# Kernel tuning notes

Hardware: AMD Instinct MI355X
Metric: run time of the kernel (lower is better)

Reference implementation:

```python
import jax, jax.numpy as jnp
import numpy as np

B, I, H = 131072, 128, 128


def _xavier(key, shape):
    fan_in, fan_out = shape
    limit = float(np.sqrt(6.0 / (fan_in + fan_out)))
    return jax.random.uniform(key, shape, jnp.float32, -limit, limit)


def setup_inputs() -> dict:
    key = jax.random.key(0)
    ks = jax.random.split(key, 12)
    inp = {
        "x_t": jax.random.normal(ks[0], (B, I), jnp.float32),
        "h_prev": jax.random.normal(ks[1], (B, H), jnp.float32),
        "c_prev": jax.random.normal(ks[2], (B, H), jnp.float32),
        "w_ii": _xavier(ks[3], (I, H)),
        "w_if": _xavier(ks[4], (I, H)),
        "w_ig": _xavier(ks[5], (I, H)),
        "w_io": _xavier(ks[6], (I, H)),
        "w_hi": _xavier(ks[7], (H, H)),
        "w_hf": _xavier(ks[8], (H, H)),
        "w_hg": _xavier(ks[9], (H, H)),
        "w_ho": _xavier(ks[10], (H, H)),
        "b_i": jnp.zeros((H,), jnp.float32),
        "b_f": jnp.zeros((H,), jnp.float32),
        "b_g": jnp.zeros((H,), jnp.float32),
        "b_o": jnp.zeros((H,), jnp.float32),
    }
    return inp


def reference(x_t, h_prev, c_prev, w_ii, w_if, w_ig, w_io,
              w_hi, w_hf, w_hg, w_ho, b_i, b_f, b_g, b_o):
    # Fused gate pre-activations: stack the 4 input and 4 hidden weight mats
    # so the 8 small GEMMs become 2 GEMMs of width 4H (same math as kernel).
    Wx = jnp.concatenate([w_ii, w_if, w_ig, w_io], axis=1)  # (I, 4H)
    Wh = jnp.concatenate([w_hi, w_hf, w_hg, w_ho], axis=1)  # (H, 4H)
    b = jnp.concatenate([b_i, b_f, b_g, b_o], axis=0)       # (4H,)
    acc = x_t @ Wx + h_prev @ Wh + b                         # (B, 4H)
    a_i, a_f, a_g, a_o = jnp.split(acc, 4, axis=1)
    i_gate = jax.nn.sigmoid(a_i)
    f_gate = jax.nn.sigmoid(a_f)
    o_gate = jax.nn.sigmoid(a_o)
    g_gate = jnp.tanh(a_g)
    c_t = f_gate * c_prev + i_gate * g_gate
    h_t = o_gate * jnp.tanh(c_t)
    return h_t, c_t
```

## Files before the change

### kernel.cpp

```cpp
#include <hip/hip_runtime.h>
#include <hip/hip_bf16.h>

#define BROWS 131072
#define HD 128

typedef __attribute__((ext_vector_type(8))) short bf16x8;
typedef __attribute__((ext_vector_type(4))) float f32x4;

static __device__ __forceinline__ unsigned short f2bf(float f) {
    union { float f; unsigned int i; } v;
    v.f = f;
    unsigned int u = v.i;
    u += 0x7FFFu + ((u >> 16) & 1u);
    return (unsigned short)(u >> 16);
}
static __device__ __forceinline__ float fast_sigmoid(float x) {
    float e = __builtin_amdgcn_exp2f(-1.442695040888963f * x);
    return __builtin_amdgcn_rcpf(1.0f + e);
}
static __device__ __forceinline__ float fast_tanh(float x) {
    float e = __builtin_amdgcn_exp2f(2.885390081777927f * x);
    return 1.0f - 2.0f * __builtin_amdgcn_rcpf(1.0f + e);
}

static __device__ __forceinline__ bf16x8 cvt8(const float* p) {
    f32x4 a = ((const f32x4*)p)[0];
    f32x4 b = ((const f32x4*)p)[1];
    __hip_bfloat162 r0 = __float22bfloat162_rn(float2{a[0], a[1]});
    __hip_bfloat162 r1 = __float22bfloat162_rn(float2{a[2], a[3]});
    __hip_bfloat162 r2 = __float22bfloat162_rn(float2{b[0], b[1]});
    __hip_bfloat162 r3 = __float22bfloat162_rn(float2{b[2], b[3]});
    union { __hip_bfloat162 h2; unsigned int u; } u0, u1, u2, u3;
    u0.h2 = r0; u1.h2 = r1; u2.h2 = r2; u3.h2 = r3;
    union { unsigned int u[4]; bf16x8 v; } out;
    out.u[0] = u0.u; out.u[1] = u1.u; out.u[2] = u2.u; out.u[3] = u3.u;
    return out.v;
}

__global__ void pack_weights(const float* __restrict__ w_ii,
                             const float* __restrict__ w_if,
                             const float* __restrict__ w_ig,
                             const float* __restrict__ w_io,
                             const float* __restrict__ w_hi,
                             const float* __restrict__ w_hf,
                             const float* __restrict__ w_hg,
                             const float* __restrict__ w_ho,
                             unsigned short* __restrict__ pack) {
    int idx = blockIdx.x * 256 + threadIdx.x;
    int n = idx & 127;
    int k = (idx >> 7) & 255;
    int g = idx >> 15;
    const float* wx = (g == 0) ? w_ii : (g == 1) ? w_if : (g == 2) ? w_ig : w_io;
    const float* wh = (g == 0) ? w_hi : (g == 1) ? w_hf : (g == 2) ? w_hg : w_ho;
    float v = (k < 128) ? wx[k * 128 + n] : wh[(k - 128) * 128 + n];
    pack[(g * 128 + n) * 256 + k] = f2bf(v);
}

__global__ __launch_bounds__(512, 4)
void lstm_main(const float* __restrict__ x,
               const float* __restrict__ h_prev,
               const float* __restrict__ c_prev,
               const unsigned short* __restrict__ pack,
               const float* __restrict__ b_i,
               const float* __restrict__ b_f,
               const float* __restrict__ b_g,
               const float* __restrict__ b_o,
               float* __restrict__ out) {
    __shared__ bf16x8 alds8[2048];
    unsigned short* alds = (unsigned short*)alds8;

    const int tid  = threadIdx.x;
    const int row0 = blockIdx.x * 64;
    const int wid  = tid >> 6;
    const int lane = tid & 63;
    const int ml   = lane & 15;
    const int q    = lane >> 4;
    const int s    = wid;

    #pragma unroll
    for (int i = 0; i < 4; ++i) {
        int c   = i * 512 + tid;
        int row = c >> 5;
        int kc  = c & 31;
        const float* src = (kc < 16) ? (x + (size_t)(row0 + row) * 128 + kc * 8)
                                     : (h_prev + (size_t)(row0 + row) * 128 + (kc - 16) * 8);
        bf16x8 v = cvt8(src);
        *((bf16x8*)&alds[row * 256 + (kc ^ (row & 7)) * 8]) = v;
    }
    __syncthreads();

    f32x4 acc[4][4];
    #pragma unroll
    for (int mt = 0; mt < 4; ++mt)
        #pragma unroll
        for (int g = 0; g < 4; ++g)
            acc[mt][g] = (f32x4){0.f, 0.f, 0.f, 0.f};

    const unsigned short* pbase = pack + ((size_t)s * 16 + ml) * 256 + q * 8;

    #pragma unroll 2
    for (int ks = 0; ks < 8; ++ks) {
        bf16x8 a[4];
        #pragma unroll
        for (int mt = 0; mt < 4; ++mt) {
            int rowl = mt * 16 + ml;
            int kcs  = (ks * 4 + q) ^ (ml & 7);
            a[mt] = *(const bf16x8*)(&alds[rowl * 256 + kcs * 8]);
        }

        bf16x8 b[4];
        #pragma unroll
        for (int g = 0; g < 4; ++g)
            b[g] = *(const bf16x8*)(pbase + (size_t)g * 8 * 16 * 256 + ks * 32);

        #pragma unroll
        for (int mt = 0; mt < 4; ++mt)
            #pragma unroll
            for (int g = 0; g < 4; ++g)
                acc[mt][g] = __builtin_amdgcn_mfma_f32_16x16x32_bf16(
                    a[mt], b[g], acc[mt][g], 0, 0, 0);
    }

    const int col = s * 16 + ml;
    float bi = b_i[col], bf_ = b_f[col], bg = b_g[col], bo = b_o[col];

    float* out_h = out;
    float* out_c = out + (size_t)BROWS * HD;

    #pragma unroll
    for (int mt = 0; mt < 4; ++mt) {
        #pragma unroll
        for (int r = 0; r < 4; ++r) {
            int row = row0 + mt * 16 + q * 4 + r;
            float ai = acc[mt][0][r] + bi;
            float af = acc[mt][1][r] + bf_;
            float ag = acc[mt][2][r] + bg;
            float ao = acc[mt][3][r] + bo;
            float ig = fast_sigmoid(ai);
            float fg = fast_sigmoid(af);
            float gg = fast_tanh(ag);
            float og = fast_sigmoid(ao);
            float cp = c_prev[(size_t)row * 128 + col];
            float cv = fg * cp + ig * gg;
            float hv = og * fast_tanh(cv);
            out_h[(size_t)row * 128 + col] = hv;
            out_c[(size_t)row * 128 + col] = cv;
        }
    }
}

extern "C" void kernel_launch(void* const* d_in, const int* in_sizes, int n_in,
                              void* d_out, int out_size, void* d_ws, size_t ws_size,
                              hipStream_t stream) {
    const float* x  = (const float*)d_in[0];
    const float* h  = (const float*)d_in[1];
    const float* c  = (const float*)d_in[2];
    unsigned short* pack = (unsigned short*)d_ws;

    pack_weights<<<512, 256, 0, stream>>>(
        (const float*)d_in[3], (const float*)d_in[4],
        (const float*)d_in[5], (const float*)d_in[6],
        (const float*)d_in[7], (const float*)d_in[8],
        (const float*)d_in[9], (const float*)d_in[10],
        pack);

    dim3 grid(BROWS / 64);
    lstm_main<<<grid, 512, 0, stream>>>(
        x, h, c, pack,
        (const float*)d_in[11], (const float*)d_in[12],
        (const float*)d_in[13], (const float*)d_in[14],
        (float*)d_out);
}
```

Baseline: 340.5 us.

## Make LSTM kernel persistent over tiles with double-buffered LDS prefetch

Each block now handles 8 consecutive 64-row tiles with 1024 threads, splitting the rows of each tile across two wave halves. The next tile's x/h data is loaded into registers during the current tile's MFMA and epilogue work, then written to the alternate LDS buffer, with c_prev loaded early. The aim is to hide global load latency behind compute and to reuse weight fetches across tiles. The trade-off is fewer blocks (256), which may leave some CUs underused, plus extra register pressure from holding staged data.

```diff
diff --git a/kernel.cpp b/kernel.cpp
--- a/kernel.cpp
+++ b/kernel.cpp
@@ -3,6 +3,7 @@
 
 #define BROWS 131072
 #define HD 128
+#define TPB 8
 
 typedef __attribute__((ext_vector_type(8))) short bf16x8;
 typedef __attribute__((ext_vector_type(4))) float f32x4;
@@ -23,9 +24,7 @@
     return 1.0f - 2.0f * __builtin_amdgcn_rcpf(1.0f + e);
 }
 
-static __device__ __forceinline__ bf16x8 cvt8(const float* p) {
-    f32x4 a = ((const f32x4*)p)[0];
-    f32x4 b = ((const f32x4*)p)[1];
+static __device__ __forceinline__ bf16x8 cvt8r(f32x4 a, f32x4 b) {
     __hip_bfloat162 r0 = __float22bfloat162_rn(float2{a[0], a[1]});
     __hip_bfloat162 r1 = __float22bfloat162_rn(float2{a[2], a[3]});
     __hip_bfloat162 r2 = __float22bfloat162_rn(float2{b[0], b[1]});
@@ -56,7 +55,7 @@
     pack[(g * 128 + n) * 256 + k] = f2bf(v);
 }
 
-__global__ __launch_bounds__(512, 4)
+__global__ __launch_bounds__(1024, 4)
 void lstm_main(const float* __restrict__ x,
                const float* __restrict__ h_prev,
                const float* __restrict__ c_prev,
@@ -66,86 +65,124 @@
                const float* __restrict__ b_g,
                const float* __restrict__ b_o,
                float* __restrict__ out) {
-    __shared__ bf16x8 alds8[2048];
-    unsigned short* alds = (unsigned short*)alds8;
+    __shared__ bf16x8 alds8[2][2048];
 
     const int tid  = threadIdx.x;
-    const int row0 = blockIdx.x * 64;
     const int wid  = tid >> 6;
     const int lane = tid & 63;
     const int ml   = lane & 15;
     const int q    = lane >> 4;
-    const int s    = wid;
-
+    const int s    = wid & 7;
+    const int mh   = wid >> 3;
+
+    const int tile0 = blockIdx.x * TPB;
+
+    int srow[2], skc[2];
     #pragma unroll
-    for (int i = 0; i < 4; ++i) {
-        int c   = i * 512 + tid;
-        int row = c >> 5;
-        int kc  = c & 31;
-        const float* src = (kc < 16) ? (x + (size_t)(row0 + row) * 128 + kc * 8)
-                                     : (h_prev + (size_t)(row0 + row) * 128 + (kc - 16) * 8);
-        bf16x8 v = cvt8(src);
-        *((bf16x8*)&alds[row * 256 + (kc ^ (row & 7)) * 8]) = v;
+    for (int i = 0; i < 2; ++i) {
+        int c = i * 1024 + tid;
+        srow[i] = c >> 5;
+        skc[i]  = c & 31;
     }
-    __syncthreads();
-
-    f32x4 acc[4][4];
-    #pragma unroll
-    for (int mt = 0; mt < 4; ++mt)
-        #pragma unroll
-        for (int g = 0; g < 4; ++g)
-            acc[mt][g] = (f32x4){0.f, 0.f, 0.f, 0.f};
+
+    f32x4 sA[2][2];
+
+    auto load_stage = [&](int t) {
+        size_t rowbase = (size_t)(tile0 + t) * 64;
+        #pragma unroll
+        for (int i = 0; i < 2; ++i) {
+            const float* src = (skc[i] < 16)
+                ? (x      + (rowbase + srow[i]) * 128 + skc[i] * 8)
+                : (h_prev + (rowbase + srow[i]) * 128 + (skc[i] - 16) * 8);
+            sA[i][0] = ((const f32x4*)src)[0];
+            sA[i][1] = ((const f32x4*)src)[1];
+        }
+    };
+    auto write_stage = [&](int buf) {
+        #pragma unroll
+        for (int i = 0; i < 2; ++i) {
+            unsigned short* dst = (unsigned short*)alds8[buf]
+                + srow[i] * 256 + (skc[i] ^ (srow[i] & 7)) * 8;
+            *(bf16x8*)dst = cvt8r(sA[i][0], sA[i][1]);
+        }
+    };
 
     const unsigned short* pbase = pack + ((size_t)s * 16 + ml) * 256 + q * 8;
-
-    #pragma unroll 2
-    for (int ks = 0; ks < 8; ++ks) {
-        bf16x8 a[4];
-        #pragma unroll
-        for (int mt = 0; mt < 4; ++mt) {
-            int rowl = mt * 16 + ml;
-            int kcs  = (ks * 4 + q) ^ (ml & 7);
-            a[mt] = *(const bf16x8*)(&alds[rowl * 256 + kcs * 8]);
-        }
-
-        bf16x8 b[4];
-        #pragma unroll
-        for (int g = 0; g < 4; ++g)
-            b[g] = *(const bf16x8*)(pbase + (size_t)g * 8 * 16 * 256 + ks * 32);
-
-        #pragma unroll
-        for (int mt = 0; mt < 4; ++mt)
-            #pragma unroll
-            for (int g = 0; g < 4; ++g)
-                acc[mt][g] = __builtin_amdgcn_mfma_f32_16x16x32_bf16(
-                    a[mt], b[g], acc[mt][g], 0, 0, 0);
-    }
-
     const int col = s * 16 + ml;
-    float bi = b_i[col], bf_ = b_f[col], bg = b_g[col], bo = b_o[col];
+    const float bi = b_i[col], bf_ = b_f[col], bg = b_g[col], bo = b_o[col];
 
     float* out_h = out;
     float* out_c = out + (size_t)BROWS * HD;
 
-    #pragma unroll
-    for (int mt = 0; mt < 4; ++mt) {
-        #pragma unroll
-        for (int r = 0; r < 4; ++r) {
-            int row = row0 + mt * 16 + q * 4 + r;
-            float ai = acc[mt][0][r] + bi;
-            float af = acc[mt][1][r] + bf_;
-            float ag = acc[mt][2][r] + bg;
-            float ao = acc[mt][3][r] + bo;
-            float ig = fast_sigmoid(ai);
-            float fg = fast_sigmoid(af);
-            float gg = fast_tanh(ag);
-            float og = fast_sigmoid(ao);
-            float cp = c_prev[(size_t)row * 128 + col];
-            float cv = fg * cp + ig * gg;
-            float hv = og * fast_tanh(cv);
-            out_h[(size_t)row * 128 + col] = hv;
-            out_c[(size_t)row * 128 + col] = cv;
-        }
+    load_stage(0);
+    write_stage(0);
+    __syncthreads();
+
+    for (int t = 0; t < TPB; ++t) {
+        const int cur = t & 1;
+
+        if (t + 1 < TPB) load_stage(t + 1);
+
+        const size_t row0 = (size_t)(tile0 + t) * 64;
+        float cp[2][4];
+        #pragma unroll
+        for (int j = 0; j < 2; ++j)
+            #pragma unroll
+            for (int r = 0; r < 4; ++r)
+                cp[j][r] = c_prev[(row0 + (mh * 2 + j) * 16 + q * 4 + r) * 128 + col];
+
+        f32x4 acc[2][4];
+        #pragma unroll
+        for (int j = 0; j < 2; ++j)
+            #pragma unroll
+            for (int g = 0; g < 4; ++g)
+                acc[j][g] = (f32x4){0.f, 0.f, 0.f, 0.f};
+
+        unsigned short* alds = (unsigned short*)alds8[cur];
+        #pragma unroll 2
+        for (int ks = 0; ks < 8; ++ks) {
+            bf16x8 a[2];
+            #pragma unroll
+            for (int j = 0; j < 2; ++j) {
+                int rowl = (mh * 2 + j) * 16 + ml;
+                int kcs  = (ks * 4 + q) ^ (ml & 7);
+                a[j] = *(const bf16x8*)(&alds[rowl * 256 + kcs * 8]);
+            }
+            bf16x8 b[4];
+            #pragma unroll
+            for (int g = 0; g < 4; ++g)
+                b[g] = *(const bf16x8*)(pbase + (size_t)g * 8 * 16 * 256 + ks * 32);
+
+            #pragma unroll
+            for (int j = 0; j < 2; ++j)
+                #pragma unroll
+                for (int g = 0; g < 4; ++g)
+                    acc[j][g] = __builtin_amdgcn_mfma_f32_16x16x32_bf16(
+                        a[j], b[g], acc[j][g], 0, 0, 0);
+        }
+
+        #pragma unroll
+        for (int j = 0; j < 2; ++j) {
+            #pragma unroll
+            for (int r = 0; r < 4; ++r) {
+                size_t row = row0 + (mh * 2 + j) * 16 + q * 4 + r;
+                float ai = acc[j][0][r] + bi;
+                float af = acc[j][1][r] + bf_;
+                float ag = acc[j][2][r] + bg;
+                float ao = acc[j][3][r] + bo;
+                float ig = fast_sigmoid(ai);
+                float fg = fast_sigmoid(af);
+                float gg = fast_tanh(ag);
+                float og = fast_sigmoid(ao);
+                float cv = fg * cp[j][r] + ig * gg;
+                float hv = og * fast_tanh(cv);
+                out_h[row * 128 + col] = hv;
+                out_c[row * 128 + col] = cv;
+            }
+        }
+
+        if (t + 1 < TPB) write_stage(cur ^ 1);
+        __syncthreads();
     }
 }
 
@@ -164,8 +201,8 @@
         (const float*)d_in[9], (const float*)d_in[10],
         pack);
 
-    dim3 grid(BROWS / 64);
-    lstm_main<<<grid, 512, 0, stream>>>(
+    dim3 grid(BROWS / (64 * TPB));
+    lstm_main<<<grid, 1024, 0, stream>>>(
         x, h, c, pack,
         (const float*)d_in[11], (const float*)d_in[12],
         (const float*)d_in[13], (const float*)d_in[14],
```

After: 407.9 us. 1.2x slower.
